# Performance work log

Measured on AMD Instinct MI355X. Metric: run time of the kernel, lower is better.

Reference implementation:

```python
import jax, jax.numpy as jnp
import numpy as np

NEG_BIG = -9e15
ALPHA = 0.2  # leakyrelu negative slope


def setup_inputs() -> dict:
    key = jax.random.key(0)
    k1, k2, k3, k4 = jax.random.split(key, 4)
    N, F_in, F_out = 8192, 256, 256
    h = jax.random.normal(k1, (N, F_in), dtype=jnp.float32)
    adj = jax.random.randint(k2, (N, N), 0, 2).astype(jnp.float32)
    W = jax.random.normal(k3, (F_in, F_out), dtype=jnp.float32) * (1.414 / np.sqrt(F_in))
    a = jax.random.normal(k4, (2 * F_out, 1), dtype=jnp.float32) * (1.414 / np.sqrt(2 * F_out))
    return {"h": h, "adj": adj, "W": W, "a": a}


def reference(h, adj, W, a):
    F_out = W.shape[1]
    Wh = h @ W  # [N, F_out]
    # Decomposed additive score: e_ij = leakyrelu(a1.Wh_i + a2.Wh_j)
    # identical to matmul(cat([Wh_i, Wh_j]), a) in the original.
    a1 = a[:F_out, 0]  # [F_out]
    a2 = a[F_out:, 0]  # [F_out]
    s1 = Wh @ a1  # [N]
    s2 = Wh @ a2  # [N]
    e = jax.nn.leaky_relu(s1[:, None] + s2[None, :], negative_slope=ALPHA)  # [N, N]
    e = jnp.where(adj > 0, e, NEG_BIG)
    attention = jax.nn.softmax(e, axis=1)
    # dropout skipped (eval mode: training=False)
    h_prime = attention @ Wh  # [N, F_out]
    return jax.nn.elu(h_prime)
```

## Files before the change

### kernel.cpp

```cpp
#include <hip/hip_runtime.h>
#include <hip/hip_bf16.h>

#define N 8192
#define F 256
#define KSPLIT 4
#define JBLK (N / KSPLIT)
#define NITER (JBLK / 64)

using s16x8 = __attribute__((ext_vector_type(8))) short;
using f32x4 = __attribute__((ext_vector_type(4))) float;

static __device__ __forceinline__ unsigned short f2bf(float f) {
  unsigned int u = __float_as_uint(f);
  unsigned int r = u + 0x7fffu + ((u >> 16) & 1u);
  return (unsigned short)(r >> 16);
}
static __device__ __forceinline__ float bf2f(unsigned short u) {
  return __uint_as_float(((unsigned int)u) << 16);
}

__global__ __launch_bounds__(256) void k0_wt(const float* __restrict__ W,
                                             unsigned short* __restrict__ Wt) {
  int k = blockIdx.x;
  int f = threadIdx.x;
  Wt[f * 256 + k] = f2bf(W[k * 256 + f]);
}

__global__ __launch_bounds__(256) void k1_wh(const float* __restrict__ h,
                                             const unsigned short* __restrict__ Wt,
                                             unsigned short* __restrict__ WhbT) {
  __shared__ char lds[8192 + 32768];
  char* Alds = lds;
  char* Blds = lds + 8192;
  int t = threadIdx.x;
  int i0 = blockIdx.x * 64;
  int l = t & 63, w = t >> 6;
  int lr = l & 15, lk = l >> 4;
  f32x4 acc[4][4] = {};
  for (int kt = 0; kt < 4; ++kt) {
    int k0 = kt * 64;
    if (kt) __syncthreads();
#pragma unroll
    for (int c = 0; c < 4; ++c) {
      int flat = c * 256 + t;
      int i = flat >> 4, jc = flat & 15;
      float4 v = *reinterpret_cast<const float4*>(h + (size_t)(i0 + i) * 256 + k0 + jc * 4);
      ushort4 pk;
      pk.x = f2bf(v.x); pk.y = f2bf(v.y); pk.z = f2bf(v.z); pk.w = f2bf(v.w);
      *reinterpret_cast<ushort4*>(Alds + i * 128 + ((jc * 8) ^ ((i & 7) << 4))) = pk;
    }
#pragma unroll
    for (int c = 0; c < 8; ++c) {
      int idx = c * 256 + t;
      int fr = idx >> 3, kc = idx & 7;
      uint4 v = *reinterpret_cast<const uint4*>(Wt + fr * 256 + k0 + kc * 8);
      *reinterpret_cast<uint4*>(Blds + fr * 128 + ((kc * 16) ^ ((fr & 7) << 4))) = v;
    }
    __syncthreads();
#pragma unroll
    for (int kk = 0; kk < 2; ++kk) {
      int kofs = kk * 64 + lk * 16;
      s16x8 afr[4], bfr[4];
#pragma unroll
      for (int mf = 0; mf < 4; ++mf) {
        int ar = mf * 16 + lr;
        afr[mf] = *reinterpret_cast<const s16x8*>(Alds + ar * 128 + (kofs ^ ((ar & 7) << 4)));
      }
#pragma unroll
      for (int nf = 0; nf < 4; ++nf) {
        int br = w * 64 + nf * 16 + lr;
        bfr[nf] = *reinterpret_cast<const s16x8*>(Blds + br * 128 + (kofs ^ ((br & 7) << 4)));
      }
#pragma unroll
      for (int mf = 0; mf < 4; ++mf)
#pragma unroll
        for (int nf = 0; nf < 4; ++nf)
          acc[mf][nf] = __builtin_amdgcn_mfma_f32_16x16x32_bf16(afr[mf], bfr[nf], acc[mf][nf], 0, 0, 0);
    }
  }
#pragma unroll
  for (int mf = 0; mf < 4; ++mf) {
#pragma unroll
    for (int nf = 0; nf < 4; ++nf) {
      int f = w * 64 + nf * 16 + lr;
      int j = i0 + mf * 16 + lk * 4;
      ushort4 pk;
      pk.x = f2bf(acc[mf][nf][0]);
      pk.y = f2bf(acc[mf][nf][1]);
      pk.z = f2bf(acc[mf][nf][2]);
      pk.w = f2bf(acc[mf][nf][3]);
      *reinterpret_cast<ushort4*>(WhbT + (size_t)f * N + j) = pk;
    }
  }
}

__global__ __launch_bounds__(256) void k2_s(const unsigned short* __restrict__ WhbT,
                                            const float* __restrict__ a,
                                            float* __restrict__ s1,
                                            float* __restrict__ s2) {
  int j = blockIdx.x * 256 + threadIdx.x;
  float acc1 = 0.f, acc2 = 0.f;
#pragma unroll 8
  for (int f = 0; f < 256; ++f) {
    float v = bf2f(WhbT[(size_t)f * N + j]);
    acc1 += v * a[f];
    acc2 += v * a[256 + f];
  }
  s1[j] = acc1;
  s2[j] = acc2;
}

__global__ __launch_bounds__(256, 2) void k3_attn(const float* __restrict__ adj,
                                                  const unsigned short* __restrict__ WhbT,
                                                  const float* __restrict__ s1,
                                                  const float* __restrict__ s2,
                                                  float* __restrict__ numw,
                                                  float* __restrict__ denw) {
  __shared__ char Bbuf[2 * 32768];
  int t = threadIdx.x;
  int wv = t >> 6;
  int l = t & 63;
  int lr = l & 15, lk = l >> 4;
  int i0 = blockIdx.x * 64;
  int ks = blockIdx.y;
  int jb = ks * JBLK;
  int row = i0 + wv * 16 + lr;
  const float* arow = adj + (size_t)row * N + jb;
  const float* s2b = s2 + jb;
  float s1v = s1[row];
  int lko = lk * 8;

  f32x4 acc[16] = {};
  float dsum = 0.f;

  float4 ajc[4], svc[4], ajn[4], svn[4];
  uint4 bvn[8];

#pragma unroll
  for (int kk = 0; kk < 2; ++kk)
#pragma unroll
    for (int h = 0; h < 2; ++h) {
      ajc[kk * 2 + h] = *reinterpret_cast<const float4*>(arow + kk * 32 + lko + h * 4);
      svc[kk * 2 + h] = *reinterpret_cast<const float4*>(s2b + kk * 32 + lko + h * 4);
    }
#pragma unroll
  for (int c = 0; c < 8; ++c) {
    int idx = c * 256 + t;
    int fr = idx >> 3, kc = idx & 7;
    bvn[c] = *reinterpret_cast<const uint4*>(WhbT + (size_t)fr * N + jb + kc * 8);
  }
#pragma unroll
  for (int c = 0; c < 8; ++c) {
    int idx = c * 256 + t;
    int fr = idx >> 3, kc = idx & 7;
    *reinterpret_cast<uint4*>(Bbuf + fr * 128 + ((kc * 16) ^ ((fr & 7) << 4))) = bvn[c];
  }
  __syncthreads();

  for (int it = 0; it < NITER; ++it) {
    bool pf = (it + 1 < NITER);
    if (pf) {
      int jn = (it + 1) * 64;
#pragma unroll
      for (int kk = 0; kk < 2; ++kk)
#pragma unroll
        for (int h = 0; h < 2; ++h)
          ajn[kk * 2 + h] = *reinterpret_cast<const float4*>(arow + jn + kk * 32 + lko + h * 4);
#pragma unroll
      for (int c = 0; c < 8; ++c) {
        int idx = c * 256 + t;
        int fr = idx >> 3, kc = idx & 7;
        bvn[c] = *reinterpret_cast<const uint4*>(WhbT + (size_t)fr * N + jb + jn + kc * 8);
      }
#pragma unroll
      for (int kk = 0; kk < 2; ++kk)
#pragma unroll
        for (int h = 0; h < 2; ++h)
          svn[kk * 2 + h] = *reinterpret_cast<const float4*>(s2b + jn + kk * 32 + lko + h * 4);
    }
    s16x8 afr[2];
#pragma unroll
    for (int kk = 0; kk < 2; ++kk) {
      unsigned short u[8];
#pragma unroll
      for (int h = 0; h < 2; ++h) {
        float4 av = ajc[kk * 2 + h];
        float4 tv = svc[kk * 2 + h];
        float x;
        x = s1v + tv.x; x = fmaxf(x, 0.2f * x); u[h * 4 + 0] = av.x > 0.f ? f2bf(__expf(x)) : 0;
        x = s1v + tv.y; x = fmaxf(x, 0.2f * x); u[h * 4 + 1] = av.y > 0.f ? f2bf(__expf(x)) : 0;
        x = s1v + tv.z; x = fmaxf(x, 0.2f * x); u[h * 4 + 2] = av.z > 0.f ? f2bf(__expf(x)) : 0;
        x = s1v + tv.w; x = fmaxf(x, 0.2f * x); u[h * 4 + 3] = av.w > 0.f ? f2bf(__expf(x)) : 0;
      }
      s16x8 af;
#pragma unroll
      for (int e = 0; e < 8; ++e) {
        af[e] = (short)u[e];
        dsum += bf2f(u[e]);
      }
      afr[kk] = af;
    }
    const char* B = Bbuf + (it & 1) * 32768;
#pragma unroll
    for (int kk = 0; kk < 2; ++kk) {
      int kofs = kk * 64 + lk * 16;
#pragma unroll
      for (int nf = 0; nf < 16; ++nf) {
        int br = nf * 16 + lr;
        s16x8 bfr = *reinterpret_cast<const s16x8*>(B + br * 128 + (kofs ^ ((br & 7) << 4)));
        acc[nf] = __builtin_amdgcn_mfma_f32_16x16x32_bf16(afr[kk], bfr, acc[nf], 0, 0, 0);
      }
    }
    if (pf) {
      char* B1 = Bbuf + ((it + 1) & 1) * 32768;
#pragma unroll
      for (int c = 0; c < 8; ++c) {
        int idx = c * 256 + t;
        int fr = idx >> 3, kc = idx & 7;
        *reinterpret_cast<uint4*>(B1 + fr * 128 + ((kc * 16) ^ ((fr & 7) << 4))) = bvn[c];
      }
    }
    __syncthreads();
    if (pf) {
#pragma unroll
      for (int q = 0; q < 4; ++q) { ajc[q] = ajn[q]; svc[q] = svn[q]; }
    }
  }

  dsum += __shfl_xor(dsum, 16);
  dsum += __shfl_xor(dsum, 32);
  if (l < 16) denw[(size_t)ks * N + row] = dsum;

  float* nump = numw + (size_t)ks * N * F;
#pragma unroll
  for (int nf = 0; nf < 16; ++nf) {
#pragma unroll
    for (int r = 0; r < 4; ++r) {
      nump[(size_t)(i0 + wv * 16 + lk * 4 + r) * F + nf * 16 + lr] = acc[nf][r];
    }
  }
}

__global__ __launch_bounds__(256) void k4_fin(const float* __restrict__ numw,
                                              const float* __restrict__ denw,
                                              float* __restrict__ out) {
  int idx = (blockIdx.x * 256 + threadIdx.x) * 4;
  int i = idx >> 8;
  float4 sn = {0.f, 0.f, 0.f, 0.f};
  float sd = 0.f;
#pragma unroll
  for (int ksp = 0; ksp < KSPLIT; ++ksp) {
    float4 v = *reinterpret_cast<const float4*>(numw + (size_t)ksp * N * F + idx);
    sn.x += v.x; sn.y += v.y; sn.z += v.z; sn.w += v.w;
    sd += denw[ksp * N + i];
  }
  float r = 1.f / sd;
  float4 o;
  float hp;
  hp = sn.x * r; o.x = hp > 0.f ? hp : (__expf(hp) - 1.f);
  hp = sn.y * r; o.y = hp > 0.f ? hp : (__expf(hp) - 1.f);
  hp = sn.z * r; o.z = hp > 0.f ? hp : (__expf(hp) - 1.f);
  hp = sn.w * r; o.w = hp > 0.f ? hp : (__expf(hp) - 1.f);
  *reinterpret_cast<float4*>(out + idx) = o;
}

extern "C" void kernel_launch(void* const* d_in, const int* in_sizes, int n_in,
                              void* d_out, int out_size, void* d_ws, size_t ws_size,
                              hipStream_t stream) {
  const float* h   = (const float*)d_in[0];
  const float* adj = (const float*)d_in[1];
  const float* W   = (const float*)d_in[2];
  const float* a   = (const float*)d_in[3];
  float* out = (float*)d_out;

  char* ws = (char*)d_ws;
  size_t o = 0;
  unsigned short* WhbT = (unsigned short*)(ws + o); o += (size_t)4 * 1024 * 1024;
  float* s1            = (float*)(ws + o); o += 32768;
  float* s2            = (float*)(ws + o); o += 32768;
  float* denw          = (float*)(ws + o); o += 131072;
  unsigned short* Wt   = (unsigned short*)(ws + o); o += 131072;
  float* numw          = (float*)(ws + o); o += (size_t)KSPLIT * N * F * 4;

  hipLaunchKernelGGL(k0_wt, dim3(256), dim3(256), 0, stream, W, Wt);
  hipLaunchKernelGGL(k1_wh, dim3(N / 64), dim3(256), 0, stream, h, Wt, WhbT);
  hipLaunchKernelGGL(k2_s, dim3(N / 256), dim3(256), 0, stream, WhbT, a, s1, s2);
  hipLaunchKernelGGL(k3_attn, dim3(128, KSPLIT), dim3(256), 0, stream,
                     adj, WhbT, s1, s2, numw, denw);
  hipLaunchKernelGGL(k4_fin, dim3(N * F / 1024), dim3(256), 0, stream, numw, denw, out);
}
```

Baseline: 146.8 us.

## Bit-pack adjacency mask, fuse score computation, tile Wh for direct-to-LDS loads

Adds a kernel that packs the fp32 adjacency matrix into a bitmask. The attention kernel then reads 1 bit per entry instead of 4 bytes, and it is read once across all row blocks. s1/s2 are now computed in the Wh GEMM epilogue and pre-scaled by log2e so exp2f can be used, which removes the separate score kernel. Wh is written in a tile-swizzled layout so the attention kernel can use global_load_lds straight into LDS. The attention kernel also processes 128 rows per block (two row fragments per wave) and raises KSPLIT to 8. The cost is an extra full read of adj in the mask kernel, larger partial-numerator buffers, and hand-written waitcnt/barrier synchronisation.

```diff
diff --git a/kernel.cpp b/kernel.cpp
--- a/kernel.cpp
+++ b/kernel.cpp
@@ -3,9 +3,10 @@
 
 #define N 8192
 #define F 256
-#define KSPLIT 4
+#define KSPLIT 8
 #define JBLK (N / KSPLIT)
 #define NITER (JBLK / 64)
+#define LOG2E 1.4426950408889634f
 
 using s16x8 = __attribute__((ext_vector_type(8))) short;
 using f32x4 = __attribute__((ext_vector_type(4))) float;
@@ -17,6 +18,36 @@
 }
 static __device__ __forceinline__ float bf2f(unsigned short u) {
   return __uint_as_float(((unsigned int)u) << 16);
+}
+static __device__ __forceinline__ void glds16(const char* g, char* l) {
+  __builtin_amdgcn_global_load_lds(
+      (const __attribute__((address_space(1))) unsigned int*)g,
+      (__attribute__((address_space(3))) unsigned int*)l, 16, 0, 0);
+}
+
+__global__ __launch_bounds__(256) void k_mask(const float* __restrict__ adj,
+                                              unsigned int* __restrict__ mask) {
+  __shared__ unsigned int nibw[8192];
+  int t = threadIdx.x;
+  for (int s = 0; s < 4; ++s) {
+    size_t chunk = (size_t)s * 2048 + blockIdx.x;
+    const float* base = adj + chunk * 8192;
+    unsigned int nib[8];
+#pragma unroll
+    for (int r = 0; r < 8; ++r) {
+      float4 v = *reinterpret_cast<const float4*>(base + (size_t)(r * 256 + t) * 4);
+      nib[r] = (v.x != 0.f ? 1u : 0u) | (v.y != 0.f ? 2u : 0u) |
+               (v.z != 0.f ? 4u : 0u) | (v.w != 0.f ? 8u : 0u);
+    }
+    if (s) __syncthreads();
+#pragma unroll
+    for (int r = 0; r < 8; ++r) nibw[r * 256 + t] = nib[r];
+    __syncthreads();
+    unsigned int wrd = 0;
+#pragma unroll
+    for (int k = 0; k < 8; ++k) wrd |= nibw[t * 8 + k] << (4 * k);
+    mask[chunk * 256 + t] = wrd;
+  }
 }
 
 __global__ __launch_bounds__(256) void k0_wt(const float* __restrict__ W,
@@ -28,7 +59,10 @@
 
 __global__ __launch_bounds__(256) void k1_wh(const float* __restrict__ h,
                                              const unsigned short* __restrict__ Wt,
-                                             unsigned short* __restrict__ WhbT) {
+                                             const float* __restrict__ a,
+                                             char* __restrict__ WhbT,
+                                             float* __restrict__ s1g,
+                                             float* __restrict__ s2g) {
   __shared__ char lds[8192 + 32768];
   char* Alds = lds;
   char* Blds = lds + 8192;
@@ -78,165 +112,178 @@
           acc[mf][nf] = __builtin_amdgcn_mfma_f32_16x16x32_bf16(afr[mf], bfr[nf], acc[mf][nf], 0, 0, 0);
     }
   }
+  int tj = blockIdx.x;
 #pragma unroll
   for (int mf = 0; mf < 4; ++mf) {
 #pragma unroll
     for (int nf = 0; nf < 4; ++nf) {
       int f = w * 64 + nf * 16 + lr;
-      int j = i0 + mf * 16 + lk * 4;
+      int jj = mf * 16 + lk * 4;
+      int kc = jj >> 3, sub = (jj >> 2) & 1;
       ushort4 pk;
       pk.x = f2bf(acc[mf][nf][0]);
       pk.y = f2bf(acc[mf][nf][1]);
       pk.z = f2bf(acc[mf][nf][2]);
       pk.w = f2bf(acc[mf][nf][3]);
-      *reinterpret_cast<ushort4*>(WhbT + (size_t)f * N + j) = pk;
-    }
-  }
-}
-
-__global__ __launch_bounds__(256) void k2_s(const unsigned short* __restrict__ WhbT,
-                                            const float* __restrict__ a,
-                                            float* __restrict__ s1,
-                                            float* __restrict__ s2) {
-  int j = blockIdx.x * 256 + threadIdx.x;
-  float acc1 = 0.f, acc2 = 0.f;
-#pragma unroll 8
-  for (int f = 0; f < 256; ++f) {
-    float v = bf2f(WhbT[(size_t)f * N + j]);
-    acc1 += v * a[f];
-    acc2 += v * a[256 + f];
-  }
-  s1[j] = acc1;
-  s2[j] = acc2;
-}
-
-__global__ __launch_bounds__(256, 2) void k3_attn(const float* __restrict__ adj,
-                                                  const unsigned short* __restrict__ WhbT,
+      *reinterpret_cast<ushort4*>(WhbT + (size_t)tj * 32768 + f * 128 +
+                                  ((kc * 16) ^ ((f & 7) << 4)) + sub * 8) = pk;
+    }
+  }
+  float a1v[4], a2v[4];
+#pragma unroll
+  for (int nf = 0; nf < 4; ++nf) {
+    int f = w * 64 + nf * 16 + lr;
+    a1v[nf] = a[f];
+    a2v[nf] = a[256 + f];
+  }
+  float* s1l = (float*)lds;
+  float* s2l = s1l + 64;
+  __syncthreads();
+  if (t < 128) s1l[t] = 0.f;
+  __syncthreads();
+#pragma unroll
+  for (int mf = 0; mf < 4; ++mf) {
+#pragma unroll
+    for (int r = 0; r < 4; ++r) {
+      float p1 = 0.f, p2 = 0.f;
+#pragma unroll
+      for (int nf = 0; nf < 4; ++nf) {
+        p1 += acc[mf][nf][r] * a1v[nf];
+        p2 += acc[mf][nf][r] * a2v[nf];
+      }
+      p1 += __shfl_xor(p1, 1); p1 += __shfl_xor(p1, 2);
+      p1 += __shfl_xor(p1, 4); p1 += __shfl_xor(p1, 8);
+      p2 += __shfl_xor(p2, 1); p2 += __shfl_xor(p2, 2);
+      p2 += __shfl_xor(p2, 4); p2 += __shfl_xor(p2, 8);
+      if (lr == 0) {
+        atomicAdd(&s1l[mf * 16 + lk * 4 + r], p1);
+        atomicAdd(&s2l[mf * 16 + lk * 4 + r], p2);
+      }
+    }
+  }
+  __syncthreads();
+  if (t < 64) {
+    s1g[i0 + t] = s1l[t] * LOG2E;
+    s2g[i0 + t] = s2l[t] * LOG2E;
+  }
+}
+
+__global__ __launch_bounds__(256, 2) void k3_attn(const unsigned char* __restrict__ mask8,
+                                                  const char* __restrict__ WhbT,
                                                   const float* __restrict__ s1,
                                                   const float* __restrict__ s2,
                                                   float* __restrict__ numw,
                                                   float* __restrict__ denw) {
-  __shared__ char Bbuf[2 * 32768];
-  int t = threadIdx.x;
-  int wv = t >> 6;
-  int l = t & 63;
-  int lr = l & 15, lk = l >> 4;
-  int i0 = blockIdx.x * 64;
+  __shared__ char lds[2 * 32768 + 4096];
+  char* Bbuf = lds;
+  float* s2l = (float*)(lds + 65536);
+  int t = threadIdx.x, w = t >> 6, l = t & 63, lr = l & 15, lk = l >> 4;
+  int i0 = blockIdx.x * 128;
   int ks = blockIdx.y;
   int jb = ks * JBLK;
-  int row = i0 + wv * 16 + lr;
-  const float* arow = adj + (size_t)row * N + jb;
-  const float* s2b = s2 + jb;
-  float s1v = s1[row];
-  int lko = lk * 8;
-
-  f32x4 acc[16] = {};
-  float dsum = 0.f;
-
-  float4 ajc[4], svc[4], ajn[4], svn[4];
-  uint4 bvn[8];
-
-#pragma unroll
-  for (int kk = 0; kk < 2; ++kk)
-#pragma unroll
-    for (int h = 0; h < 2; ++h) {
-      ajc[kk * 2 + h] = *reinterpret_cast<const float4*>(arow + kk * 32 + lko + h * 4);
-      svc[kk * 2 + h] = *reinterpret_cast<const float4*>(s2b + kk * 32 + lko + h * 4);
-    }
-#pragma unroll
-  for (int c = 0; c < 8; ++c) {
-    int idx = c * 256 + t;
-    int fr = idx >> 3, kc = idx & 7;
-    bvn[c] = *reinterpret_cast<const uint4*>(WhbT + (size_t)fr * N + jb + kc * 8);
-  }
-#pragma unroll
-  for (int c = 0; c < 8; ++c) {
-    int idx = c * 256 + t;
-    int fr = idx >> 3, kc = idx & 7;
-    *reinterpret_cast<uint4*>(Bbuf + fr * 128 + ((kc * 16) ^ ((fr & 7) << 4))) = bvn[c];
-  }
-  __syncthreads();
+
+  {
+    float4 v = *reinterpret_cast<const float4*>(s2 + jb + t * 4);
+    *reinterpret_cast<float4*>(s2l + t * 4) = v;
+  }
+  int row0 = i0 + w * 32 + lr;
+  int row1 = row0 + 16;
+  float s1p0 = s1[row0], s1p1 = s1[row1];
+  const unsigned char* mr0 = mask8 + (size_t)row0 * (N / 8) + (jb >> 3);
+  const unsigned char* mr1 = mask8 + (size_t)row1 * (N / 8) + (jb >> 3);
+
+  f32x4 acc[2][16] = {};
+  float ds0 = 0.f, ds1 = 0.f;
+
+#define GLDS_TILE(tile, buf)                                                  \
+  {                                                                           \
+    const char* gsrc = WhbT + ((size_t)(ks * NITER + (tile))) * 32768;        \
+    char* ldst = Bbuf + (buf) * 32768;                                        \
+    _Pragma("unroll") for (int c = 0; c < 8; ++c)                             \
+        glds16(gsrc + c * 4096 + w * 1024 + l * 16, ldst + c * 4096 + w * 1024); \
+  }
+
+  unsigned int mb0a = mr0[lk], mb0b = mr0[4 + lk];
+  unsigned int mb1a = mr1[lk], mb1b = mr1[4 + lk];
+  GLDS_TILE(0, 0);
 
   for (int it = 0; it < NITER; ++it) {
-    bool pf = (it + 1 < NITER);
+    int cb = it & 1;
+    bool pf = (it + 1) < NITER;
+    unsigned int nb0a = 0, nb0b = 0, nb1a = 0, nb1b = 0;
     if (pf) {
-      int jn = (it + 1) * 64;
-#pragma unroll
-      for (int kk = 0; kk < 2; ++kk)
-#pragma unroll
-        for (int h = 0; h < 2; ++h)
-          ajn[kk * 2 + h] = *reinterpret_cast<const float4*>(arow + jn + kk * 32 + lko + h * 4);
-#pragma unroll
-      for (int c = 0; c < 8; ++c) {
-        int idx = c * 256 + t;
-        int fr = idx >> 3, kc = idx & 7;
-        bvn[c] = *reinterpret_cast<const uint4*>(WhbT + (size_t)fr * N + jb + jn + kc * 8);
-      }
-#pragma unroll
-      for (int kk = 0; kk < 2; ++kk)
-#pragma unroll
-        for (int h = 0; h < 2; ++h)
-          svn[kk * 2 + h] = *reinterpret_cast<const float4*>(s2b + jn + kk * 32 + lko + h * 4);
-    }
-    s16x8 afr[2];
-#pragma unroll
-    for (int kk = 0; kk < 2; ++kk) {
-      unsigned short u[8];
-#pragma unroll
-      for (int h = 0; h < 2; ++h) {
-        float4 av = ajc[kk * 2 + h];
-        float4 tv = svc[kk * 2 + h];
-        float x;
-        x = s1v + tv.x; x = fmaxf(x, 0.2f * x); u[h * 4 + 0] = av.x > 0.f ? f2bf(__expf(x)) : 0;
-        x = s1v + tv.y; x = fmaxf(x, 0.2f * x); u[h * 4 + 1] = av.y > 0.f ? f2bf(__expf(x)) : 0;
-        x = s1v + tv.z; x = fmaxf(x, 0.2f * x); u[h * 4 + 2] = av.z > 0.f ? f2bf(__expf(x)) : 0;
-        x = s1v + tv.w; x = fmaxf(x, 0.2f * x); u[h * 4 + 3] = av.w > 0.f ? f2bf(__expf(x)) : 0;
-      }
-      s16x8 af;
-#pragma unroll
-      for (int e = 0; e < 8; ++e) {
-        af[e] = (short)u[e];
-        dsum += bf2f(u[e]);
-      }
-      afr[kk] = af;
-    }
-    const char* B = Bbuf + (it & 1) * 32768;
+      int o = (it + 1) * 8;
+      nb0a = mr0[o + lk]; nb0b = mr0[o + 4 + lk];
+      nb1a = mr1[o + lk]; nb1b = mr1[o + 4 + lk];
+      GLDS_TILE(it + 1, cb ^ 1);
+      asm volatile("s_waitcnt vmcnt(8)" ::: "memory");
+    } else {
+      asm volatile("s_waitcnt vmcnt(0)" ::: "memory");
+    }
+    asm volatile("s_waitcnt lgkmcnt(0)" ::: "memory");
+    __builtin_amdgcn_s_barrier();
+
+    s16x8 af00, af01, af10, af11;
+    {
+      int jofs = it * 64 + lk * 8;
+      float4 sa0 = *reinterpret_cast<const float4*>(s2l + jofs);
+      float4 sb0 = *reinterpret_cast<const float4*>(s2l + jofs + 4);
+      float4 sa1 = *reinterpret_cast<const float4*>(s2l + jofs + 32);
+      float4 sb1 = *reinterpret_cast<const float4*>(s2l + jofs + 36);
+#define PEL(dst, e, s1p, sv, mv, dsx)                                         \
+      {                                                                       \
+        float x = (s1p) + (sv); x = fmaxf(x, 0.2f * x);                       \
+        float p = ((mv >> (e)) & 1u) ? exp2f(x) : 0.f;                        \
+        unsigned short us = (unsigned short)((__float_as_uint(p) + 0x8000u) >> 16); \
+        dsx += bf2f(us); dst[e] = (short)us;                                  \
+      }
+#define PFRAG(dst, s1p, sa, sb, mv, dsx)                                      \
+      PEL(dst, 0, s1p, sa.x, mv, dsx) PEL(dst, 1, s1p, sa.y, mv, dsx)         \
+      PEL(dst, 2, s1p, sa.z, mv, dsx) PEL(dst, 3, s1p, sa.w, mv, dsx)         \
+      PEL(dst, 4, s1p, sb.x, mv, dsx) PEL(dst, 5, s1p, sb.y, mv, dsx)         \
+      PEL(dst, 6, s1p, sb.z, mv, dsx) PEL(dst, 7, s1p, sb.w, mv, dsx)
+      PFRAG(af00, s1p0, sa0, sb0, mb0a, ds0)
+      PFRAG(af01, s1p0, sa1, sb1, mb0b, ds0)
+      PFRAG(af10, s1p1, sa0, sb0, mb1a, ds1)
+      PFRAG(af11, s1p1, sa1, sb1, mb1b, ds1)
+#undef PFRAG
+#undef PEL
+    }
+    const char* B = Bbuf + cb * 32768;
 #pragma unroll
     for (int kk = 0; kk < 2; ++kk) {
       int kofs = kk * 64 + lk * 16;
+      s16x8 a0 = kk ? af01 : af00;
+      s16x8 a1 = kk ? af11 : af10;
 #pragma unroll
       for (int nf = 0; nf < 16; ++nf) {
         int br = nf * 16 + lr;
         s16x8 bfr = *reinterpret_cast<const s16x8*>(B + br * 128 + (kofs ^ ((br & 7) << 4)));
-        acc[nf] = __builtin_amdgcn_mfma_f32_16x16x32_bf16(afr[kk], bfr, acc[nf], 0, 0, 0);
-      }
-    }
-    if (pf) {
-      char* B1 = Bbuf + ((it + 1) & 1) * 32768;
-#pragma unroll
-      for (int c = 0; c < 8; ++c) {
-        int idx = c * 256 + t;
-        int fr = idx >> 3, kc = idx & 7;
-        *reinterpret_cast<uint4*>(B1 + fr * 128 + ((kc * 16) ^ ((fr & 7) << 4))) = bvn[c];
-      }
-    }
-    __syncthreads();
-    if (pf) {
-#pragma unroll
-      for (int q = 0; q < 4; ++q) { ajc[q] = ajn[q]; svc[q] = svn[q]; }
-    }
-  }
-
-  dsum += __shfl_xor(dsum, 16);
-  dsum += __shfl_xor(dsum, 32);
-  if (l < 16) denw[(size_t)ks * N + row] = dsum;
-
+        acc[0][nf] = __builtin_amdgcn_mfma_f32_16x16x32_bf16(a0, bfr, acc[0][nf], 0, 0, 0);
+        acc[1][nf] = __builtin_amdgcn_mfma_f32_16x16x32_bf16(a1, bfr, acc[1][nf], 0, 0, 0);
+      }
+    }
+    asm volatile("s_waitcnt lgkmcnt(0)" ::: "memory");
+    __builtin_amdgcn_s_barrier();
+    mb0a = nb0a; mb0b = nb0b; mb1a = nb1a; mb1b = nb1b;
+  }
+#undef GLDS_TILE
+
+  ds0 += __shfl_xor(ds0, 16); ds0 += __shfl_xor(ds0, 32);
+  ds1 += __shfl_xor(ds1, 16); ds1 += __shfl_xor(ds1, 32);
+  if (l < 16) {
+    denw[(size_t)ks * N + row0] = ds0;
+    denw[(size_t)ks * N + row1] = ds1;
+  }
   float* nump = numw + (size_t)ks * N * F;
 #pragma unroll
-  for (int nf = 0; nf < 16; ++nf) {
-#pragma unroll
-    for (int r = 0; r < 4; ++r) {
-      nump[(size_t)(i0 + wv * 16 + lk * 4 + r) * F + nf * 16 + lr] = acc[nf][r];
+  for (int mf = 0; mf < 2; ++mf) {
+#pragma unroll
+    for (int nf = 0; nf < 16; ++nf) {
+#pragma unroll
+      for (int r = 0; r < 4; ++r) {
+        nump[(size_t)(i0 + w * 32 + mf * 16 + lk * 4 + r) * F + nf * 16 + lr] = acc[mf][nf][r];
+      }
     }
   }
 }
@@ -252,7 +299,7 @@
   for (int ksp = 0; ksp < KSPLIT; ++ksp) {
     float4 v = *reinterpret_cast<const float4*>(numw + (size_t)ksp * N * F + idx);
     sn.x += v.x; sn.y += v.y; sn.z += v.z; sn.w += v.w;
-    sd += denw[ksp * N + i];
+    sd += denw[(size_t)ksp * N + i];
   }
   float r = 1.f / sd;
   float4 o;
@@ -275,17 +322,18 @@
 
   char* ws = (char*)d_ws;
   size_t o = 0;
-  unsigned short* WhbT = (unsigned short*)(ws + o); o += (size_t)4 * 1024 * 1024;
-  float* s1            = (float*)(ws + o); o += 32768;
-  float* s2            = (float*)(ws + o); o += 32768;
-  float* denw          = (float*)(ws + o); o += 131072;
-  unsigned short* Wt   = (unsigned short*)(ws + o); o += 131072;
-  float* numw          = (float*)(ws + o); o += (size_t)KSPLIT * N * F * 4;
-
+  char* WhbT           = ws + o;                        o += (size_t)4 * 1024 * 1024;
+  float* s1            = (float*)(ws + o);              o += 32768;
+  float* s2            = (float*)(ws + o);              o += 32768;
+  float* denw          = (float*)(ws + o);              o += (size_t)KSPLIT * N * 4;
+  unsigned short* Wt   = (unsigned short*)(ws + o);     o += 131072;
+  unsigned int* mask   = (unsigned int*)(ws + o);       o += (size_t)N * (N / 32) * 4;
+  float* numw          = (float*)(ws + o);              o += (size_t)KSPLIT * N * F * 4;
+
+  hipLaunchKernelGGL(k_mask, dim3(2048), dim3(256), 0, stream, adj, mask);
   hipLaunchKernelGGL(k0_wt, dim3(256), dim3(256), 0, stream, W, Wt);
-  hipLaunchKernelGGL(k1_wh, dim3(N / 64), dim3(256), 0, stream, h, Wt, WhbT);
-  hipLaunchKernelGGL(k2_s, dim3(N / 256), dim3(256), 0, stream, WhbT, a, s1, s2);
-  hipLaunchKernelGGL(k3_attn, dim3(128, KSPLIT), dim3(256), 0, stream,
-                     adj, WhbT, s1, s2, numw, denw);
+  hipLaunchKernelGGL(k1_wh, dim3(N / 64), dim3(256), 0, stream, h, Wt, a, WhbT, s1, s2);
+  hipLaunchKernelGGL(k3_attn, dim3(N / 128, KSPLIT), dim3(256), 0, stream,
+                     (const unsigned char*)mask, WhbT, s1, s2, numw, denw);
   hipLaunchKernelGGL(k4_fin, dim3(N * F / 1024), dim3(256), 0, stream, numw, denw, out);
 }
```

Result: slower. 155.2 us (+5.7%).
